# Performance work log

Hardware: AMD Instinct MI355X
Metric: run time of the kernel (lower is better)

The kernel has to match this reference:

```python
import jax, jax.numpy as jnp
import numpy as np

D_MODEL = 2048
N_HEADS = 16
N_KV_HEADS = 4
HEAD_DIM = 128
ROPE_THETA = 1000000.0
B, T = 2, 2048


def setup_inputs() -> dict:
    key = jax.random.key(0)
    ks = jax.random.split(key, 5)
    s_in = 1.0 / np.sqrt(D_MODEL)
    s_o = 1.0 / np.sqrt(N_HEADS * HEAD_DIM)
    return {
        "x": jax.random.normal(ks[0], (B, T, D_MODEL), jnp.float32),
        "w_q": jax.random.normal(ks[1], (N_HEADS * HEAD_DIM, D_MODEL), jnp.float32) * s_in,
        "w_k": jax.random.normal(ks[2], (N_KV_HEADS * HEAD_DIM, D_MODEL), jnp.float32) * s_in,
        "w_v": jax.random.normal(ks[3], (N_KV_HEADS * HEAD_DIM, D_MODEL), jnp.float32) * s_in,
        "w_o": jax.random.normal(ks[4], (D_MODEL, N_HEADS * HEAD_DIM), jnp.float32) * s_o,
    }


def _rope_cos_sin(T, dtype):
    # inv_freq over even dims, emb = concat(freqs, freqs) (HF/llama convention)
    inv_freq = 1.0 / (ROPE_THETA ** (jnp.arange(0, HEAD_DIM, 2, dtype=jnp.float32) / HEAD_DIM))
    freqs = jnp.arange(T, dtype=jnp.float32)[:, None] * inv_freq[None, :]  # [T, hd/2]
    emb = jnp.concatenate([freqs, freqs], axis=-1)  # [T, hd]
    return jnp.cos(emb).astype(dtype), jnp.sin(emb).astype(dtype)


def _rotate_half(x):
    x1, x2 = jnp.split(x, 2, axis=-1)
    return jnp.concatenate([-x2, x1], axis=-1)


def reference(x, w_q, w_k, w_v, w_o):
    B, T, D = x.shape
    # QKV projections (bias=False), split heads -> [B, H, T, hd]
    q = (x @ w_q.T).reshape(B, T, N_HEADS, HEAD_DIM).transpose(0, 2, 1, 3)
    k = (x @ w_k.T).reshape(B, T, N_KV_HEADS, HEAD_DIM).transpose(0, 2, 1, 3)
    v = (x @ w_v.T).reshape(B, T, N_KV_HEADS, HEAD_DIM).transpose(0, 2, 1, 3)
    # RoPE
    cos, sin = _rope_cos_sin(T, x.dtype)  # [T, hd]
    q = q * cos + _rotate_half(q) * sin
    k = k * cos + _rotate_half(k) * sin
    # GQA: expand kv heads (repeat_interleave over head dim)
    rep = N_HEADS // N_KV_HEADS
    k = jnp.repeat(k, rep, axis=1)
    v = jnp.repeat(v, rep, axis=1)
    # Eager attention: QK^T * scale + causal mask, softmax, PV
    scale = HEAD_DIM ** -0.5
    scores = jnp.einsum("bhtd,bhsd->bhts", q, k) * scale
    causal = jnp.tril(jnp.ones((T, T), dtype=bool))
    scores = jnp.where(causal[None, None], scores, jnp.finfo(scores.dtype).min)
    probs = jax.nn.softmax(scores, axis=-1)
    out = jnp.einsum("bhts,bhsd->bhtd", probs, v)  # [B, H, T, hd]
    out = out.transpose(0, 2, 1, 3).reshape(B, T, N_HEADS * HEAD_DIM)
    return out @ w_o.T
```

## Files before the change

kernel.cpp:

```cpp
#include <hip/hip_runtime.h>
#include <cstdint>
#include <cstddef>

typedef unsigned short u16;
typedef unsigned u32;
typedef unsigned long long u64;
typedef __attribute__((ext_vector_type(8))) short short8;
typedef __attribute__((ext_vector_type(4))) float f32x4;

#define T_SEQ 2048
#define DM    2048
#define NHEAD 16
#define NKV   4
#define HD    128
#define NEGBIG (-3.0e38f)
#define QSCALE 0.1275525165017459f
#define L2IF (-0.31143258583318043f)

__device__ __forceinline__ u16 f2bf(float f) {
  union { float f; unsigned u; } c; c.f = f;
  return (u16)((c.u + 0x7fffu + ((c.u >> 16) & 1u)) >> 16);
}
__device__ __forceinline__ float bf2f(u16 b) {
  union { float f; unsigned u; } c; c.u = ((unsigned)b) << 16;
  return c.f;
}
__device__ __forceinline__ void gl_lds16(const u16* g, u16* l) {
  __builtin_amdgcn_global_load_lds(
      (const __attribute__((address_space(1))) void*)g,
      (__attribute__((address_space(3))) void*)l, 16, 0, 0);
}

#define FENCE() asm volatile("" ::: "memory")
#define BAR() do { FENCE(); __builtin_amdgcn_s_barrier(); FENCE(); } while (0)
#define WAITV4() asm volatile("s_waitcnt vmcnt(4)" ::: "memory")
#define WAITV0() asm volatile("s_waitcnt vmcnt(0)" ::: "memory")

__global__ void castk_all(const float* __restrict__ x, const float* __restrict__ wq,
                          const float* __restrict__ wk, const float* __restrict__ wv,
                          const float* __restrict__ wo, u16* __restrict__ dst) {
  long long i4 = (long long)blockIdx.x * 256 + threadIdx.x;
  const float* src; long long off;
  if (i4 < (2LL << 20))                    { src = x;  off = i4; }
  else if (i4 < (3LL << 20))               { src = wq; off = i4 - (2LL << 20); }
  else if (i4 < (3LL << 20) + (1 << 18))   { src = wk; off = i4 - (3LL << 20); }
  else if (i4 < (3LL << 20) + (2 << 18))   { src = wv; off = i4 - (3LL << 20) - (1 << 18); }
  else                                     { src = wo; off = i4 - (3LL << 20) - (2 << 18); }
  float4 v = *(const float4*)(src + off * 4);
  u16* d = dst + i4 * 4;
  d[0] = f2bf(v.x); d[1] = f2bf(v.y); d[2] = f2bf(v.z); d[3] = f2bf(v.w);
}

__global__ void tabk(float2* __restrict__ Tab) {
  int idx = blockIdx.x * 256 + threadIdx.x;
  float ang = (float)(idx >> 6) * exp2f((float)(idx & 63) * L2IF);
  float sn, cs;
  sincosf(ang, &sn, &cs);
  Tab[idx] = make_float2(cs, sn);
}

__global__ void ropek(u16* __restrict__ buf, const float2* __restrict__ Tab) {
  int idx = blockIdx.x * 256 + threadIdx.x;
  int r = idx >> 6, i = idx & 63;
  int t = r & (T_SEQ - 1);
  float2 cs = Tab[(t << 6) + i];
  size_t base = (size_t)r * HD + i;
  float x1 = bf2f(buf[base]), x2 = bf2f(buf[base + 64]);
  buf[base]      = f2bf(x1 * cs.x - x2 * cs.y);
  buf[base + 64] = f2bf(x2 * cs.x + x1 * cs.y);
}

template <int FH>
__device__ __forceinline__ void mfma_quad(f32x4 (&acc)[8][4], const short8 (&af)[4],
                                          const short8 (&bfr)[4]) {
#pragma unroll
  for (int i = 0; i < 4; ++i)
#pragma unroll
    for (int j = 0; j < 4; ++j)
      acc[FH * 4 + i][j] =
          __builtin_amdgcn_mfma_f32_16x16x32_bf16(af[i], bfr[j], acc[FH * 4 + i][j], 0, 0, 0);
}

template <int MODE>
__global__ __launch_bounds__(512, 2) void gemm8(
    const u16* __restrict__ A, const u16* __restrict__ Bm,
    void* __restrict__ Out0, u16* __restrict__ OutK, u16* __restrict__ OutV,
    int M, int N, int K) {
  __shared__ __align__(16) u16 AS[2][2][256 * 32];
  __shared__ __align__(16) u16 BS[2][2][256 * 32];
  const int tid = threadIdx.x;
  const int l = tid & 63, lm = l & 15, q = l >> 4;
  const int w = tid >> 6, wr = w >> 2, wc = w & 3;
  const int m0 = blockIdx.y * 256, n0 = blockIdx.x * 256;
  const u16* Ab = A + (size_t)m0 * K;
  const u16* Bb = Bm + (size_t)n0 * K;

  const int r0 = tid >> 2, c0 = (tid & 3) * 8;
  const int r1 = (512 + tid) >> 2, c1 = (tid & 3) * 8;

#define STG_A(T, KC) do { \
    const int kb_ = (T) * 64 + (KC) * 32; \
    gl_lds16(Ab + (size_t)r0 * K + kb_ + c0, &AS[(T) & 1][KC][tid * 8]); \
    gl_lds16(Ab + (size_t)r1 * K + kb_ + c1, &AS[(T) & 1][KC][(512 + tid) * 8]); \
  } while (0)
#define STG_B(T, KC) do { \
    const int kb_ = (T) * 64 + (KC) * 32; \
    gl_lds16(Bb + (size_t)r0 * K + kb_ + c0, &BS[(T) & 1][KC][tid * 8]); \
    gl_lds16(Bb + (size_t)r1 * K + kb_ + c1, &BS[(T) & 1][KC][(512 + tid) * 8]); \
  } while (0)

  f32x4 acc[8][4] = {};
  const int nt = K >> 6;

  STG_A(0, 0); STG_B(0, 0);
  STG_A(0, 1); STG_B(0, 1);
  STG_A(1, 0); STG_B(1, 0);
  WAITV4();
  BAR();

  for (int t = 0; t < nt; ++t) {
    const int cur = t & 1;
    short8 bfr[4];

    {
      short8 af[4];
#pragma unroll
      for (int i = 0; i < 4; ++i)
        bfr[i] = *(const short8*)(&BS[cur][0][(wc * 64 + i * 16 + lm) * 32 + q * 8]);
#pragma unroll
      for (int i = 0; i < 4; ++i)
        af[i] = *(const short8*)(&AS[cur][0][(wr * 128 + i * 16 + lm) * 32 + q * 8]);
      if (t + 1 < nt) { STG_A(t + 1, 1); STG_B(t + 1, 1); }
      BAR();
      __builtin_amdgcn_s_setprio(1);
      mfma_quad<0>(acc, af, bfr);
      __builtin_amdgcn_s_setprio(0);
      BAR();
    }
    {
      short8 af[4];
#pragma unroll
      for (int i = 0; i < 4; ++i)
        af[i] = *(const short8*)(&AS[cur][0][(wr * 128 + (4 + i) * 16 + lm) * 32 + q * 8]);
      BAR();
      __builtin_amdgcn_s_setprio(1);
      mfma_quad<1>(acc, af, bfr);
      __builtin_amdgcn_s_setprio(0);
      BAR();
    }
    {
      short8 af[4];
#pragma unroll
      for (int i = 0; i < 4; ++i)
        bfr[i] = *(const short8*)(&BS[cur][1][(wc * 64 + i * 16 + lm) * 32 + q * 8]);
#pragma unroll
      for (int i = 0; i < 4; ++i)
        af[i] = *(const short8*)(&AS[cur][1][(wr * 128 + i * 16 + lm) * 32 + q * 8]);
      if (t + 2 < nt) STG_A(t + 2, 0);
      BAR();
      __builtin_amdgcn_s_setprio(1);
      mfma_quad<0>(acc, af, bfr);
      __builtin_amdgcn_s_setprio(0);
      BAR();
    }
    {
      short8 af[4];
#pragma unroll
      for (int i = 0; i < 4; ++i)
        af[i] = *(const short8*)(&AS[cur][1][(wr * 128 + (4 + i) * 16 + lm) * 32 + q * 8]);
      if (t + 2 < nt) STG_B(t + 2, 0);
      BAR();
      __builtin_amdgcn_s_setprio(1);
      mfma_quad<1>(acc, af, bfr);
      __builtin_amdgcn_s_setprio(0);
      if (t < nt - 2) { WAITV4(); } else { WAITV0(); }
      BAR();
    }
  }
#undef STG_A
#undef STG_B

#pragma unroll
  for (int fm = 0; fm < 8; ++fm)
#pragma unroll
    for (int fn = 0; fn < 4; ++fn)
#pragma unroll
      for (int r = 0; r < 4; ++r) {
        int m = m0 + wr * 128 + fm * 16 + q * 4 + r;
        int n = n0 + wc * 64 + fn * 16 + lm;
        float v = acc[fm][fn][r];
        if constexpr (MODE == 0) {
          ((float*)Out0)[(size_t)m * N + n] = v;
        } else {
          int b = m >> 11, tt = m & (T_SEQ - 1);
          if (n < 2048) {
            int h = n >> 7, d = n & (HD - 1);
            ((u16*)Out0)[(((size_t)(b * NHEAD + h)) * T_SEQ + tt) * HD + d] = f2bf(v * QSCALE);
          } else if (n < 2560) {
            int nn = n - 2048, h = nn >> 7, d = nn & (HD - 1);
            OutK[(((size_t)(b * NKV + h)) * T_SEQ + tt) * HD + d] = f2bf(v);
          } else {
            int nn = n - 2560, h = nn >> 7, d = nn & (HD - 1);
            OutV[(((size_t)(b * NKV + h)) * HD + d) * T_SEQ + tt] = f2bf(v);
          }
        }
      }
}

#define PSTRIDE 72
__global__ __launch_bounds__(256, 2) void attnk(
    const u16* __restrict__ Q, const u16* __restrict__ Kh,
    const u16* __restrict__ Vt, const float2* __restrict__ Tab,
    u16* __restrict__ Oa) {
  __shared__ __align__(16) u16 Ks[2][64 * 128];
  __shared__ __align__(16) u16 Vs[2][128 * 64];
  __shared__ __align__(16) u16 Pl[4][16 * PSTRIDE];
  const int tid = threadIdx.x;
  const int w = tid >> 6, l = tid & 63, lm = l & 15, q = l >> 4;

  const int wg = blockIdx.x;
  const int g = wg & 7, slot = wg >> 3;
  const int b = g >> 2, kvh = g & 3;
  const int h = kvh * 4 + (slot & 3);
  const int p = slot >> 2;

  const u16* Kb = Kh + ((size_t)(b * NKV + kvh)) * T_SEQ * HD;
  const u16* Vb = Vt + ((size_t)(b * NKV + kvh)) * HD * T_SEQ;
  u16* Pw = Pl[w];

  const int r16 = tid >> 4, c16 = tid & 15;
  const int r8  = tid >> 3, c8  = tid & 7;

#pragma unroll 1
  for (int half = 0; half < 2; ++half) {
    const int tile = half ? p : (31 - p);
    const int tbase = tile * 64 + w * 16;
    const u16* Qb = Q + (((size_t)(b * NHEAD + h)) * T_SEQ + tbase) * HD;

    short8 qa[4];
#pragma unroll
    for (int ks = 0; ks < 4; ++ks)
      qa[ks] = *(const short8*)(Qb + (size_t)lm * HD + ks * 32 + q * 8);

    {
      const float2* tb = Tab + (((size_t)(tbase + lm)) << 6) + q * 8;
#pragma unroll
      for (int ks = 0; ks < 2; ++ks) {
        short8 lo = qa[ks], hi = qa[ks + 2];
#pragma unroll
        for (int e = 0; e < 8; ++e) {
          float2 cs = tb[ks * 32 + e];
          float x1 = bf2f((u16)lo[e]), x2 = bf2f((u16)hi[e]);
          lo[e] = (short)f2bf(x1 * cs.x - x2 * cs.y);
          hi[e] = (short)f2bf(x2 * cs.x + x1 * cs.y);
        }
        qa[ks] = lo; qa[ks + 2] = hi;
      }
    }

    float m_i = NEGBIG, l_i = 0.f;
    f32x4 oacc[8] = {};
    const int nst = tile + 1;

    {
#pragma unroll
      for (int j = 0; j < 4; ++j) {
        int s = j * 16 + r16, gs = c16 ^ (s & 15);
        gl_lds16(Kb + (size_t)s * HD + gs * 8, &Ks[0][s * 128 + c16 * 8]);
      }
#pragma unroll
      for (int j = 0; j < 4; ++j) {
        int d = j * 32 + r8, gs = c8 ^ (d & 7);
        gl_lds16(Vb + (size_t)d * T_SEQ + gs * 8, &Vs[0][d * 64 + c8 * 8]);
      }
    }
    __syncthreads();

    for (int st = 0; st < nst; ++st) {
      const int bb = st & 1;
      if (st + 1 < nst) {
        const int s0n = (st + 1) * 64;
#pragma unroll
        for (int j = 0; j < 4; ++j) {
          int s = j * 16 + r16, gs = c16 ^ (s & 15);
          gl_lds16(Kb + (size_t)(s0n + s) * HD + gs * 8, &Ks[bb ^ 1][s * 128 + c16 * 8]);
        }
#pragma unroll
        for (int j = 0; j < 4; ++j) {
          int d = j * 32 + r8, gs = c8 ^ (d & 7);
          gl_lds16(Vb + (size_t)d * T_SEQ + s0n + gs * 8, &Vs[bb ^ 1][d * 64 + c8 * 8]);
        }
      }

      f32x4 sacc[4] = {};
#pragma unroll
      for (int ks = 0; ks < 4; ++ks)
#pragma unroll
        for (int nt = 0; nt < 4; ++nt) {
          short8 kb = *(const short8*)(&Ks[bb][(nt * 16 + lm) * 128 + ((ks * 4 + q) ^ lm) * 8]);
          sacc[nt] = __builtin_amdgcn_mfma_f32_16x16x32_bf16(kb, qa[ks], sacc[nt], 0, 0, 0);
        }

      const bool diag = (st == nst - 1);
      const int s0 = st * 64;
      float mx = NEGBIG;
#pragma unroll
      for (int nt = 0; nt < 4; ++nt)
#pragma unroll
        for (int j = 0; j < 4; ++j) {
          float v = sacc[nt][j];
          if (diag) {
            int s_abs = s0 + nt * 16 + q * 4 + j;
            if (s_abs > tbase + lm) v = NEGBIG;
            sacc[nt][j] = v;
          }
          mx = fmaxf(mx, v);
        }
      mx = fmaxf(mx, __shfl_xor(mx, 16, 64));
      mx = fmaxf(mx, __shfl_xor(mx, 32, 64));
      if (__any(mx > m_i + 8.0f)) {
        float mnew = fmaxf(m_i, mx);
        float alpha = exp2f(m_i - mnew);
        m_i = mnew;
        l_i *= alpha;
#pragma unroll
        for (int dt = 0; dt < 8; ++dt)
#pragma unroll
          for (int j = 0; j < 4; ++j) oacc[dt][j] *= alpha;
      }
      float sum = 0.f;
#pragma unroll
      for (int nt = 0; nt < 4; ++nt) {
        float e0 = exp2f(sacc[nt][0] - m_i), e1 = exp2f(sacc[nt][1] - m_i);
        float e2 = exp2f(sacc[nt][2] - m_i), e3 = exp2f(sacc[nt][3] - m_i);
        sum += (e0 + e1) + (e2 + e3);
        u32 lo32 = __builtin_amdgcn_perm(__float_as_uint(e1), __float_as_uint(e0), 0x07060302u);
        u32 hi32 = __builtin_amdgcn_perm(__float_as_uint(e3), __float_as_uint(e2), 0x07060302u);
        *(u64*)(Pw + lm * PSTRIDE + nt * 16 + q * 4) = ((u64)hi32 << 32) | lo32;
      }
      sum += __shfl_xor(sum, 16, 64);
      sum += __shfl_xor(sum, 32, 64);
      l_i += sum;

      asm volatile("" ::: "memory");

#pragma unroll
      for (int ks = 0; ks < 2; ++ks) {
        short8 pa = *(const short8*)(Pw + lm * PSTRIDE + ks * 32 + q * 8);
#pragma unroll
        for (int dt = 0; dt < 8; ++dt) {
          short8 vb = *(const short8*)(
              &Vs[bb][(dt * 16 + lm) * 64 + ((ks * 4 + q) ^ (lm & 7)) * 8]);
          oacc[dt] = __builtin_amdgcn_mfma_f32_16x16x32_bf16(vb, pa, oacc[dt], 0, 0, 0);
        }
      }
      __syncthreads();
    }

    float inv = 1.0f / l_i;
    int t = tbase + lm;
#pragma unroll
    for (int dt = 0; dt < 8; ++dt) {
      u16 ok[4];
#pragma unroll
      for (int j = 0; j < 4; ++j) ok[j] = f2bf(oacc[dt][j] * inv);
      *(u64*)(Oa + ((size_t)(b * T_SEQ + t)) * (NHEAD * HD) + h * HD + dt * 16 + q * 4) =
          (u64)ok[0] | ((u64)ok[1] << 16) | ((u64)ok[2] << 32) | ((u64)ok[3] << 48);
    }
  }
}

extern "C" void kernel_launch(void* const* d_in, const int* in_sizes, int n_in,
                              void* d_out, int out_size, void* d_ws, size_t ws_size,
                              hipStream_t stream) {
  const float* x  = (const float*)d_in[0];
  const float* wq = (const float*)d_in[1];
  const float* wk = (const float*)d_in[2];
  const float* wv = (const float*)d_in[3];
  const float* wo = (const float*)d_in[4];
  float* out = (float*)d_out;

  u16* ws  = (u16*)d_ws;
  u16* xb  = ws;
  u16* wqb = xb  + (8u << 20);
  u16* wkb = wqb + (4u << 20);
  u16* wvb = wkb + (1u << 20);
  u16* wob = wvb + (1u << 20);
  u16* Qb  = wob + (4u << 20);
  u16* Kb  = Qb  + (8u << 20);
  u16* Vtb = Kb  + (2u << 20);
  u16* Ab  = xb;
  float2* tab = (float2*)wkb;

  castk_all<<<18432, 256, 0, stream>>>(x, wq, wk, wv, wo, ws);

  gemm8<3><<<dim3(12, 16), 512, 0, stream>>>(xb, wqb, Qb, Kb, Vtb, 4096, 3072, 2048);

  tabk<<<512, 256, 0, stream>>>(tab);
  ropek<<<4096, 256, 0, stream>>>(Kb, tab);

  attnk<<<512, 256, 0, stream>>>(Qb, Kb, Vtb, tab, Ab);

  gemm8<0><<<dim3(8, 16), 512, 0, stream>>>(Ab, wob, out, nullptr, nullptr, 4096, 2048, 2048);
}
```

Baseline: 332.8 us.

## Swizzle GEMM LDS layout, split staging loads, add smaller-tile output projection GEMM

The GEMM staging now writes an XOR-swizzled column layout into LDS, and fragment reads apply the matching swizzle to reduce LDS bank conflicts. In the QKV GEMM, the next-tile B staging moves to the second sub-step so global loads are spread more evenly. The output projection switches to a new 128x256-tile kernel, giving 256 workgroups instead of 128 so the GPU's compute units are better covered. The trade-off is lower per-block data reuse in that kernel and more complex wait-count bookkeeping.

```diff
diff --git a/kernel.cpp b/kernel.cpp
--- a/kernel.cpp
+++ b/kernel.cpp
@@ -34,6 +34,7 @@
 #define FENCE() asm volatile("" ::: "memory")
 #define BAR() do { FENCE(); __builtin_amdgcn_s_barrier(); FENCE(); } while (0)
 #define WAITV4() asm volatile("s_waitcnt vmcnt(4)" ::: "memory")
+#define WAITV3() asm volatile("s_waitcnt vmcnt(3)" ::: "memory")
 #define WAITV0() asm volatile("s_waitcnt vmcnt(0)" ::: "memory")
 
 __global__ void castk_all(const float* __restrict__ x, const float* __restrict__ wq,
@@ -70,6 +71,7 @@
   buf[base + 64] = f2bf(x2 * cs.x + x1 * cs.y);
 }
 
+
 template <int FH>
 __device__ __forceinline__ void mfma_quad(f32x4 (&acc)[8][4], const short8 (&af)[4],
                                           const short8 (&bfr)[4]) {
@@ -95,18 +97,19 @@
   const u16* Ab = A + (size_t)m0 * K;
   const u16* Bb = Bm + (size_t)n0 * K;
 
-  const int r0 = tid >> 2, c0 = (tid & 3) * 8;
-  const int r1 = (512 + tid) >> 2, c1 = (tid & 3) * 8;
+  const int r0 = tid >> 2, r1 = 128 + (tid >> 2);
+  const int sc = (((tid & 3) ^ ((tid >> 3) & 3))) * 8;
+  const int rs = (lm >> 1) & 3;
 
 #define STG_A(T, KC) do { \
     const int kb_ = (T) * 64 + (KC) * 32; \
-    gl_lds16(Ab + (size_t)r0 * K + kb_ + c0, &AS[(T) & 1][KC][tid * 8]); \
-    gl_lds16(Ab + (size_t)r1 * K + kb_ + c1, &AS[(T) & 1][KC][(512 + tid) * 8]); \
+    gl_lds16(Ab + (size_t)r0 * K + kb_ + sc, &AS[(T) & 1][KC][tid * 8]); \
+    gl_lds16(Ab + (size_t)r1 * K + kb_ + sc, &AS[(T) & 1][KC][(512 + tid) * 8]); \
   } while (0)
 #define STG_B(T, KC) do { \
     const int kb_ = (T) * 64 + (KC) * 32; \
-    gl_lds16(Bb + (size_t)r0 * K + kb_ + c0, &BS[(T) & 1][KC][tid * 8]); \
-    gl_lds16(Bb + (size_t)r1 * K + kb_ + c1, &BS[(T) & 1][KC][(512 + tid) * 8]); \
+    gl_lds16(Bb + (size_t)r0 * K + kb_ + sc, &BS[(T) & 1][KC][tid * 8]); \
+    gl_lds16(Bb + (size_t)r1 * K + kb_ + sc, &BS[(T) & 1][KC][(512 + tid) * 8]); \
   } while (0)
 
   f32x4 acc[8][4] = {};
@@ -126,11 +129,11 @@
       short8 af[4];
 #pragma unroll
       for (int i = 0; i < 4; ++i)
-        bfr[i] = *(const short8*)(&BS[cur][0][(wc * 64 + i * 16 + lm) * 32 + q * 8]);
-#pragma unroll
-      for (int i = 0; i < 4; ++i)
-        af[i] = *(const short8*)(&AS[cur][0][(wr * 128 + i * 16 + lm) * 32 + q * 8]);
-      if (t + 1 < nt) { STG_A(t + 1, 1); STG_B(t + 1, 1); }
+        bfr[i] = *(const short8*)(&BS[cur][0][(wc * 64 + i * 16 + lm) * 32 + (q ^ rs) * 8]);
+#pragma unroll
+      for (int i = 0; i < 4; ++i)
+        af[i] = *(const short8*)(&AS[cur][0][(wr * 128 + i * 16 + lm) * 32 + (q ^ rs) * 8]);
+      if (t + 1 < nt) STG_A(t + 1, 1);
       BAR();
       __builtin_amdgcn_s_setprio(1);
       mfma_quad<0>(acc, af, bfr);
@@ -141,7 +144,8 @@
       short8 af[4];
 #pragma unroll
       for (int i = 0; i < 4; ++i)
-        af[i] = *(const short8*)(&AS[cur][0][(wr * 128 + (4 + i) * 16 + lm) * 32 + q * 8]);
+        af[i] = *(const short8*)(&AS[cur][0][(wr * 128 + (4 + i) * 16 + lm) * 32 + (q ^ rs) * 8]);
+      if (t + 1 < nt) STG_B(t + 1, 1);
       BAR();
       __builtin_amdgcn_s_setprio(1);
       mfma_quad<1>(acc, af, bfr);
@@ -152,10 +156,10 @@
       short8 af[4];
 #pragma unroll
       for (int i = 0; i < 4; ++i)
-        bfr[i] = *(const short8*)(&BS[cur][1][(wc * 64 + i * 16 + lm) * 32 + q * 8]);
-#pragma unroll
-      for (int i = 0; i < 4; ++i)
-        af[i] = *(const short8*)(&AS[cur][1][(wr * 128 + i * 16 + lm) * 32 + q * 8]);
+        bfr[i] = *(const short8*)(&BS[cur][1][(wc * 64 + i * 16 + lm) * 32 + (q ^ rs) * 8]);
+#pragma unroll
+      for (int i = 0; i < 4; ++i)
+        af[i] = *(const short8*)(&AS[cur][1][(wr * 128 + i * 16 + lm) * 32 + (q ^ rs) * 8]);
       if (t + 2 < nt) STG_A(t + 2, 0);
       BAR();
       __builtin_amdgcn_s_setprio(1);
@@ -167,7 +171,7 @@
       short8 af[4];
 #pragma unroll
       for (int i = 0; i < 4; ++i)
-        af[i] = *(const short8*)(&AS[cur][1][(wr * 128 + (4 + i) * 16 + lm) * 32 + q * 8]);
+        af[i] = *(const short8*)(&AS[cur][1][(wr * 128 + (4 + i) * 16 + lm) * 32 + (q ^ rs) * 8]);
       if (t + 2 < nt) STG_B(t + 2, 0);
       BAR();
       __builtin_amdgcn_s_setprio(1);
@@ -207,6 +211,96 @@
       }
 }
 
+__global__ __launch_bounds__(512, 2) void gemm8n(
+    const u16* __restrict__ A, const u16* __restrict__ Bm,
+    float* __restrict__ Out, int M, int N, int K) {
+  __shared__ __align__(16) u16 AS[2][2][128 * 32];
+  __shared__ __align__(16) u16 BS[2][2][256 * 32];
+  const int tid = threadIdx.x;
+  const int l = tid & 63, lm = l & 15, q = l >> 4;
+  const int w = tid >> 6, wr = w >> 2, wc = w & 3;
+  const int m0 = blockIdx.y * 128, n0 = blockIdx.x * 256;
+  const u16* Ab = A + (size_t)m0 * K;
+  const u16* Bb = Bm + (size_t)n0 * K;
+
+  const int r0 = tid >> 2, r1 = 128 + (tid >> 2);
+  const int sc = (((tid & 3) ^ ((tid >> 3) & 3))) * 8;
+  const int rs = (lm >> 1) & 3;
+
+#define STG_A(T, KC) \
+    gl_lds16(Ab + (size_t)r0 * K + (T) * 64 + (KC) * 32 + sc, &AS[(T) & 1][KC][tid * 8])
+#define STG_B(T, KC) do { \
+    const int kb_ = (T) * 64 + (KC) * 32; \
+    gl_lds16(Bb + (size_t)r0 * K + kb_ + sc, &BS[(T) & 1][KC][tid * 8]); \
+    gl_lds16(Bb + (size_t)r1 * K + kb_ + sc, &BS[(T) & 1][KC][(512 + tid) * 8]); \
+  } while (0)
+
+  f32x4 acc[4][4] = {};
+  const int nt = K >> 6;
+
+  STG_A(0, 0); STG_B(0, 0);
+  STG_A(0, 1); STG_B(0, 1);
+  STG_A(1, 0); STG_B(1, 0);
+  WAITV3();
+  BAR();
+
+  for (int t = 0; t < nt; ++t) {
+    const int cur = t & 1;
+    {
+      short8 af[4], bfr[4];
+#pragma unroll
+      for (int i = 0; i < 4; ++i)
+        bfr[i] = *(const short8*)(&BS[cur][0][(wc * 64 + i * 16 + lm) * 32 + (q ^ rs) * 8]);
+#pragma unroll
+      for (int i = 0; i < 4; ++i)
+        af[i] = *(const short8*)(&AS[cur][0][(wr * 64 + i * 16 + lm) * 32 + (q ^ rs) * 8]);
+      if (t + 1 < nt) { STG_A(t + 1, 1); STG_B(t + 1, 1); }
+      BAR();
+      __builtin_amdgcn_s_setprio(1);
+#pragma unroll
+      for (int i = 0; i < 4; ++i)
+#pragma unroll
+        for (int j = 0; j < 4; ++j)
+          acc[i][j] = __builtin_amdgcn_mfma_f32_16x16x32_bf16(af[i], bfr[j], acc[i][j], 0, 0, 0);
+      __builtin_amdgcn_s_setprio(0);
+      BAR();
+    }
+    {
+      short8 af[4], bfr[4];
+#pragma unroll
+      for (int i = 0; i < 4; ++i)
+        bfr[i] = *(const short8*)(&BS[cur][1][(wc * 64 + i * 16 + lm) * 32 + (q ^ rs) * 8]);
+#pragma unroll
+      for (int i = 0; i < 4; ++i)
+        af[i] = *(const short8*)(&AS[cur][1][(wr * 64 + i * 16 + lm) * 32 + (q ^ rs) * 8]);
+      if (t + 2 < nt) { STG_A(t + 2, 0); STG_B(t + 2, 0); }
+      BAR();
+      __builtin_amdgcn_s_setprio(1);
+#pragma unroll
+      for (int i = 0; i < 4; ++i)
+#pragma unroll
+        for (int j = 0; j < 4; ++j)
+          acc[i][j] = __builtin_amdgcn_mfma_f32_16x16x32_bf16(af[i], bfr[j], acc[i][j], 0, 0, 0);
+      __builtin_amdgcn_s_setprio(0);
+      if (t < nt - 2) { WAITV3(); } else { WAITV0(); }
+      BAR();
+    }
+  }
+#undef STG_A
+#undef STG_B
+
+#pragma unroll
+  for (int fm = 0; fm < 4; ++fm)
+#pragma unroll
+    for (int fn = 0; fn < 4; ++fn)
+#pragma unroll
+      for (int r = 0; r < 4; ++r) {
+        int m = m0 + wr * 64 + fm * 16 + q * 4 + r;
+        int n = n0 + wc * 64 + fn * 16 + lm;
+        Out[(size_t)m * N + n] = acc[fm][fn][r];
+      }
+}
+
 #define PSTRIDE 72
 __global__ __launch_bounds__(256, 2) void attnk(
     const u16* __restrict__ Q, const u16* __restrict__ Kh,
@@ -401,5 +495,5 @@
 
   attnk<<<512, 256, 0, stream>>>(Qb, Kb, Vtb, tab, Ab);
 
-  gemm8<0><<<dim3(8, 16), 512, 0, stream>>>(Ab, wob, out, nullptr, nullptr, 4096, 2048, 2048);
-}
+  gemm8n<<<dim3(8, 32), 512, 0, stream>>>(Ab, wob, out, 4096, 2048, 2048);
+}
```

Measured after the change: 316.4 us. -4.9%, faster.
